# Kernel optimization log

Hardware: AMD Instinct MI355X
Metric: run time of the kernel (lower is better)

Reference implementation:

```python
import jax, jax.numpy as jnp
import numpy as np
import math

D_MODEL = 1024
EXPAND = 2
D_INNER = D_MODEL * EXPAND  # 2048
D_STATE = 16
DT_RANK = max(1, (D_MODEL + 15) // 16)  # 64
K = 4  # conv kernel size
B, S = 2, 2048


def silu(v):
    return v * jax.nn.sigmoid(v)


def setup_inputs() -> dict:
    key = jax.random.key(0)
    ks = jax.random.split(key, 12)
    sc = lambda fan_in: 1.0 / math.sqrt(fan_in)
    x = jax.random.normal(ks[0], (B, S, D_MODEL), dtype=jnp.float32)
    Win = jax.random.normal(ks[1], (D_MODEL, 2 * D_INNER), dtype=jnp.float32) * sc(D_MODEL)
    Wconv = jax.random.normal(ks[2], (D_INNER, 1, K), dtype=jnp.float32) * sc(K)
    bconv = jax.random.normal(ks[3], (D_INNER,), dtype=jnp.float32) * 0.01
    Wx = jax.random.normal(ks[4], (D_INNER, DT_RANK + 2 * D_STATE), dtype=jnp.float32) * sc(D_INNER)
    Wdt = jax.random.normal(ks[5], (DT_RANK, D_INNER), dtype=jnp.float32) * sc(DT_RANK)
    # dt_proj bias init: inverse-softplus of dt ~ LogUniform[1e-3, 1e-1]
    dt = jnp.exp(jax.random.uniform(ks[6], (D_INNER,)) * (math.log(0.1) - math.log(0.001)) + math.log(0.001))
    dt = jnp.clip(dt, 0.0001, None)
    bdt = dt + jnp.log(-jnp.expm1(-dt))
    a = jnp.arange(1, D_STATE + 1, dtype=jnp.float32)[None, :].repeat(D_INNER, axis=0)
    a = a + jax.random.uniform(ks[7], a.shape) * 0.1
    A_log = jnp.log(a)
    Dp = jnp.ones((D_INNER,), dtype=jnp.float32)
    Wout = jax.random.normal(ks[8], (D_INNER, D_MODEL), dtype=jnp.float32) * sc(D_INNER)
    return {"x": x, "Win": Win, "Wconv": Wconv, "bconv": bconv, "Wx": Wx,
            "Wdt": Wdt, "bdt": bdt, "A_log": A_log, "Dp": Dp, "Wout": Wout}


def causal_dw_conv(x, Wconv, bconv):
    # x: [B, S, C] -> depthwise causal conv along S
    xc = jnp.transpose(x, (0, 2, 1))  # [B, C, S]
    y = jax.lax.conv_general_dilated(
        xc, Wconv, window_strides=(1,), padding=[(K - 1, 0)],
        feature_group_count=D_INNER,
        dimension_numbers=("NCH", "OIH", "NCH"))
    y = y + bconv[None, :, None]
    return jnp.transpose(y, (0, 2, 1))  # [B, S, C]


def selective_scan(u, delta, b_term, c_term, A_log, Dp):
    # u, delta: [B,S,Di]; b_term, c_term: [B,S,Ds]
    a = -jnp.exp(A_log)  # [Di, Ds]
    delta_a = jnp.exp(delta[..., None] * a[None, None])            # [B,S,Di,Ds] fp32
    delta_b_u = (delta * u)[..., None] * b_term[:, :, None, :]     # [B,S,Di,Ds]
    du = u * Dp[None, None, :]                                     # [B,S,Di]
    # time-major for scan
    dA = jnp.transpose(delta_a, (1, 0, 2, 3))
    dBu = jnp.transpose(delta_b_u, (1, 0, 2, 3))
    c_t = jnp.transpose(c_term, (1, 0, 2))
    du_t = jnp.transpose(du, (1, 0, 2))

    def step(state, inp):
        dA_t, dBu_t, c, duv = inp
        state = dA_t * state + dBu_t                  # [B,Di,Ds]
        y = jnp.einsum("bdn,bn->bd", state, c) + duv  # [B,Di]
        return state, y

    init = jnp.zeros((u.shape[0], D_INNER, D_STATE), dtype=jnp.float32)
    _, ys = jax.lax.scan(step, init, (dA, dBu, c_t, du_t))
    return jnp.transpose(ys, (1, 0, 2))  # [B,S,Di]


def reference(x, Win, Wconv, bconv, Wx, Wdt, bdt, A_log, Dp, Wout):
    xz = x @ Win                              # [B,S,2*Di]
    x_branch, z_branch = jnp.split(xz, 2, axis=-1)
    x_branch = silu(causal_dw_conv(x_branch, Wconv, bconv))
    params = x_branch @ Wx                    # [B,S,R+2*Ds]
    delta, b_term, c_term = jnp.split(params, [DT_RANK, DT_RANK + D_STATE], axis=-1)
    delta = jax.nn.softplus(delta @ Wdt + bdt)
    y = selective_scan(x_branch, delta, b_term, c_term, A_log, Dp)
    y = y * silu(z_branch)
    return y @ Wout
```

## Files before the change

### kernel.cpp

```cpp
#include <hip/hip_runtime.h>

typedef unsigned short u16;
typedef _Float16 f16;
typedef f16 f16x8 __attribute__((ext_vector_type(8)));
typedef u16 u16x8 __attribute__((ext_vector_type(8)));
typedef short s16x8 __attribute__((ext_vector_type(8)));
typedef float f32x4 __attribute__((ext_vector_type(4)));
typedef float f32x8 __attribute__((ext_vector_type(8)));

#define T_TOK 4096
#define B_SZ 2
#define S_LEN 2048
#define DMODEL 1024
#define DI 2048
#define DS 16
#define RNK 64
#define NCH 64
#define CLEN 32
#define LDXZ 4096
#define SK 8
#define PRM_SLICE (4096 * 128)
#define LOG2E 1.4426950408889634f

#define GLOAD_LDS16(gp, lp)                                                                   \
  __builtin_amdgcn_global_load_lds((const __attribute__((address_space(1))) void*)(gp),       \
                                   (__attribute__((address_space(3))) void*)(lp), 16, 0, 0)

__device__ __forceinline__ float b2f(u16 v) { return __uint_as_float(((unsigned)v) << 16); }
__device__ __forceinline__ u16 f2b(float f) {
  unsigned u = __float_as_uint(f);
  return (u16)((u + 0x7fffu + ((u >> 16) & 1u)) >> 16);
}
__device__ __forceinline__ float fexp2(float x) {
#if __has_builtin(__builtin_amdgcn_exp2f)
  return __builtin_amdgcn_exp2f(x);
#else
  return exp2f(x);
#endif
}
__device__ __forceinline__ int dtype_of(const void* dp) {
  unsigned v = *(const unsigned*)dp;
  return (v == 0x3F800000u) ? 0 : (v == 0x3C003C00u) ? 2 : 1;
}
__device__ __forceinline__ float load_any(const void* p, size_t i, int flag) {
  if (flag == 0) return ((const float*)p)[i];
  if (flag == 1) return b2f(((const u16*)p)[i]);
  return (float)((const f16*)p)[i];
}

__device__ __forceinline__ void tr_tile(const void* __restrict__ src, void* __restrict__ dst,
                                        int R, int C, int Cpad, int f, int bx, int by, int ob) {
  __shared__ f16 t[32][33];
  int c0 = bx * 32, r0 = by * 32;
  int tx = threadIdx.x & 31, ty = threadIdx.x >> 5;
#pragma unroll
  for (int i = ty; i < 32; i += 8) {
    int r = r0 + i, c = c0 + tx;
    float v = (r < R && c < C) ? load_any(src, (size_t)r * C + c, f) : 0.f;
    t[i][tx] = (f16)v;
  }
  __syncthreads();
#pragma unroll
  for (int i = ty; i < 32; i += 8) {
    int c = c0 + i, r = r0 + tx;
    if (c < Cpad && r < R) {
      if (ob) ((u16*)dst)[(size_t)c * R + r] = f2b((float)t[tx][i]);
      else ((f16*)dst)[(size_t)c * R + r] = t[tx][i];
    }
  }
}

__global__ __launch_bounds__(256) void k_prep(const void* __restrict__ Wconv, const void* __restrict__ bconv,
                                              const void* __restrict__ bdt, const void* __restrict__ A_log,
                                              const void* __restrict__ Dp, const void* __restrict__ Wx,
                                              const void* __restrict__ Wdt, const void* __restrict__ Win,
                                              const void* __restrict__ x, f16* __restrict__ WxT,
                                              f16* __restrict__ WdtT, u16* __restrict__ WinTb,
                                              u16* __restrict__ xhb, float* __restrict__ a_f,
                                              float* __restrict__ wconv_f, float* __restrict__ bconv_f,
                                              float* __restrict__ bdt_f, float* __restrict__ dp_f,
                                              int* __restrict__ flag) {
  int f = dtype_of(Dp);
  int bid = blockIdx.x, t = threadIdx.x;
  if (bid < 128) {
    int i = bid * 256 + t;
    a_f[i] = -__expf(load_any(A_log, i, f)) * LOG2E;
  } else if (bid < 160) {
    int i = (bid - 128) * 256 + t;
    wconv_f[i] = load_any(Wconv, i, f);
  } else if (bid < 168) {
    int i = (bid - 160) * 256 + t;
    bconv_f[i] = load_any(bconv, i, f);
  } else if (bid < 176) {
    int i = (bid - 168) * 256 + t;
    bdt_f[i] = load_any(bdt, i, f);
  } else if (bid < 184) {
    int i = (bid - 176) * 256 + t;
    dp_f[i] = load_any(Dp, i, f);
  } else if (bid == 184) {
    if (t == 0) *flag = f;
  } else if (bid < 441) {
    int id = bid - 185;
    tr_tile(Wx, WxT, 2048, 96, 128, f, id & 3, id >> 2, 0);
  } else if (bid < 569) {
    int id = bid - 441;
    tr_tile(Wdt, WdtT, 64, 2048, 2048, f, id & 63, id >> 6, 0);
  } else if (bid < 4665) {
    int id = bid - 569;
    tr_tile(Win, WinTb, 1024, 4096, 4096, f, id & 127, id >> 7, 1);
  } else {
    if (f == 1) return;
    size_t i = (size_t)(bid - 4665) * 2048 + (size_t)t * 8;
    u16x8 o;
    if (f == 0) {
      const float* s = (const float*)x + i;
#pragma unroll
      for (int j = 0; j < 8; ++j) o[j] = f2b(s[j]);
    } else {
      const f16* s = (const f16*)x + i;
#pragma unroll
      for (int j = 0; j < 8; ++j) o[j] = f2b((float)s[j]);
    }
    *(u16x8*)(xhb + i) = o;
  }
}

__global__ __launch_bounds__(256) void k_transpose16(const void* __restrict__ src, f16* __restrict__ dst,
                                                     int R, int C, int Cpad, const void* __restrict__ Dp) {
  tr_tile(src, dst, R, C, Cpad, dtype_of(Dp), blockIdx.x, blockIdx.y, 0);
}

__global__ __launch_bounds__(512) void k_gemm1(const void* __restrict__ x0, const u16* __restrict__ xhb,
                                               const u16* __restrict__ Bw, f16* __restrict__ C,
                                               const int* __restrict__ flag) {
  constexpr int LD = 1024, LDC = LDXZ, NT = 16, NP = NT / 2;
  __shared__ __align__(16) u16 lds[8 * 8192];
  const u16* A = (*flag == 1) ? (const u16*)x0 : xhb;
  const int tid = threadIdx.x;
  const int wv = tid >> 6, ln = tid & 63;
  const int quad = ln >> 4, l16 = ln & 15;
  const int wr = wv >> 2, wc = wv & 3;
  const int m0 = blockIdx.y * 256, n0 = blockIdx.x * 256;
  const int rr = tid >> 3;
  const int cc = (tid & 7) ^ (rr & 7);
  const u16* aBase = A + (size_t)m0 * LD + cc * 8;
  const u16* bBase = Bw + (size_t)n0 * LD + cc * 8;
  const int brow = ((tid >> 8) << 6) + (rr & 31);
  u16* const dBase = lds + wv * 512;
  auto stageA = [&](int tile, int mq) {
    const u16* s = aBase + (size_t)(mq * 64 + rr) * LD + tile * 64;
    u16* d = dBase + ((tile & 1) * 4 + mq) * 8192;
    GLOAD_LDS16(s, d);
    GLOAD_LDS16(s + 128 * LD, d + 4096);
  };
  auto stageB = [&](int tile, int nq) {
    const u16* s = bBase + (size_t)(brow + nq * 32) * LD + tile * 64;
    u16* d = dBase + ((tile & 1) * 4 + 2 + nq) * 8192;
    GLOAD_LDS16(s, d);
    GLOAD_LDS16(s + 128 * LD, d + 4096);
  };
  const int rxor = (l16 & 7) << 3;
  f32x4 acc[8][4] = {};
  stageA(0, 0); stageB(0, 1); stageB(0, 0); stageA(0, 1);
  stageA(1, 0); stageB(1, 1);
  asm volatile("s_waitcnt vmcnt(4)" ::: "memory");
  __builtin_amdgcn_s_barrier();
  s16x8 af[4][2], bf[2][2];
  for (int pr = 0; pr < NP; ++pr) {
    const int t0 = 2 * pr;
    const bool more = (pr < NP - 1);
#pragma unroll
    for (int ph = 0; ph < 8; ++ph) {
      const int slot = ph >> 2, q = ph & 3;
      const int mq = q >> 1, nq = (q >> 1) ^ (q & 1);
      const u16* Ar = lds + (slot * 4 + mq) * 8192;
      const u16* Br = lds + (slot * 4 + 2 + nq) * 8192;
      if (q == 0 || q == 2) {
#pragma unroll
        for (int i = 0; i < 4; ++i) {
          const int ra = wr * 64 + i * 16 + l16;
#pragma unroll
          for (int kk = 0; kk < 2; ++kk)
            af[i][kk] = *(const s16x8*)(Ar + ra * 64 + ((kk * 32 + quad * 8) ^ rxor));
        }
      }
      if (q != 2) {
#pragma unroll
        for (int j = 0; j < 2; ++j) {
          const int rb = wc * 32 + j * 16 + l16;
#pragma unroll
          for (int kk = 0; kk < 2; ++kk)
            bf[j][kk] = *(const s16x8*)(Br + rb * 64 + ((kk * 32 + quad * 8) ^ rxor));
        }
      }
      if (ph == 0) stageB(t0 + 1, 0);
      else if (ph == 1) stageA(t0 + 1, 1);
      else if (more) {
        if (ph == 2) stageA(t0 + 2, 0);
        else if (ph == 3) stageB(t0 + 2, 1);
        else if (ph == 4) stageB(t0 + 2, 0);
        else if (ph == 5) stageA(t0 + 2, 1);
        else if (ph == 6) stageA(t0 + 3, 0);
        else stageB(t0 + 3, 1);
      }
      __builtin_amdgcn_s_barrier();
      asm volatile("s_waitcnt lgkmcnt(0)" ::: "memory");
      __builtin_amdgcn_sched_barrier(0);
      __builtin_amdgcn_s_setprio(1);
#pragma unroll
      for (int kk = 0; kk < 2; ++kk)
#pragma unroll
        for (int i = 0; i < 4; ++i)
#pragma unroll
          for (int j = 0; j < 2; ++j)
            acc[mq * 4 + i][nq * 2 + j] = __builtin_amdgcn_mfma_f32_16x16x32_bf16(
                af[i][kk], bf[j][kk], acc[mq * 4 + i][nq * 2 + j], 0, 0, 0);
      __builtin_amdgcn_s_setprio(0);
      if (ph == 3) {
        if (more) asm volatile("s_waitcnt vmcnt(6)" ::: "memory");
        else asm volatile("s_waitcnt vmcnt(2)" ::: "memory");
      } else if (ph == 5) {
        if (more) asm volatile("s_waitcnt vmcnt(8)" ::: "memory");
        else asm volatile("s_waitcnt vmcnt(0)" ::: "memory");
      } else if (ph == 7) {
        if (more) asm volatile("s_waitcnt vmcnt(4)" ::: "memory");
        else asm volatile("s_waitcnt vmcnt(0)" ::: "memory");
      }
      __builtin_amdgcn_s_barrier();
    }
  }
#pragma unroll
  for (int i = 0; i < 8; ++i)
#pragma unroll
    for (int j = 0; j < 4; ++j)
#pragma unroll
      for (int r = 0; r < 4; ++r) {
        const int row = m0 + wr * 128 + i * 16 + quad * 4 + r;
        const int col = n0 + wc * 64 + j * 16 + l16;
        C[(size_t)row * LDC + col] = (f16)acc[i][j][r];
      }
}

template <int BM, int BN, int EPI>
__global__ __launch_bounds__(256) void k_gemm2(const f16* __restrict__ A, const f16* __restrict__ B,
                                               void* __restrict__ Cv, const float* __restrict__ bias,
                                               const int* __restrict__ flag,
                                               int klen, int lda, int ldb, int ldc) {
  constexpr int WM = BM / 2, WN = BN / 2;
  constexpr int FM = WM / 16, FN = WN / 16;
  __shared__ __align__(16) f16 As[2 * BM * 32];
  __shared__ __align__(16) f16 Bs[2 * BN * 32];
  const int tid = threadIdx.x;
  const int wv = tid >> 6, ln = tid & 63;
  const int quad = ln >> 4, l16 = ln & 15;
  const int lrow = ln >> 2, lch = (ln & 3) * 8;
  const int m0 = blockIdx.y * BM, n0 = blockIdx.x * BN;
  const int wm = (wv & 1) * WM, wn = (wv >> 1) * WN;
  const int kbase = blockIdx.z * klen;
  f32x4 acc[FM][FN] = {};
  for (int kk = 0; kk < klen; kk += 64) {
    const int k0 = kbase + kk;
    __syncthreads();
#pragma unroll
    for (int h = 0; h < 2; ++h) {
#pragma unroll
      for (int i = 0; i < BM / 64; ++i) {
        int r0 = wv * (BM / 4) + i * 16;
        GLOAD_LDS16(A + (size_t)(m0 + r0 + lrow) * lda + k0 + h * 32 + lch, As + h * BM * 32 + r0 * 32);
      }
#pragma unroll
      for (int i = 0; i < BN / 64; ++i) {
        int r0 = wv * (BN / 4) + i * 16;
        GLOAD_LDS16(B + (size_t)(n0 + r0 + lrow) * ldb + k0 + h * 32 + lch, Bs + h * BN * 32 + r0 * 32);
      }
    }
    __syncthreads();
#pragma unroll
    for (int h = 0; h < 2; ++h) {
      f16x8 af[FM], bf[FN];
#pragma unroll
      for (int i = 0; i < FM; ++i) af[i] = *(const f16x8*)(As + h * BM * 32 + (wm + i * 16 + l16) * 32 + quad * 8);
#pragma unroll
      for (int j = 0; j < FN; ++j) bf[j] = *(const f16x8*)(Bs + h * BN * 32 + (wn + j * 16 + l16) * 32 + quad * 8);
#pragma unroll
      for (int i = 0; i < FM; ++i)
#pragma unroll
        for (int j = 0; j < FN; ++j)
          acc[i][j] = __builtin_amdgcn_mfma_f32_16x16x32_f16(af[i], bf[j], acc[i][j], 0, 0, 0);
    }
  }
  int dflag = 1;
  if constexpr (EPI == 2) dflag = *flag;
  f16* Cz = (f16*)Cv;
  if constexpr (EPI == 4) Cz = (f16*)Cv + (size_t)blockIdx.z * PRM_SLICE;
#pragma unroll
  for (int i = 0; i < FM; ++i)
#pragma unroll
    for (int j = 0; j < FN; ++j)
#pragma unroll
      for (int r = 0; r < 4; ++r) {
        int row = m0 + wm + i * 16 + quad * 4 + r;
        int col = n0 + wn + j * 16 + l16;
        size_t ci = (size_t)row * ldc + col;
        float v = acc[i][j][r];
        if constexpr (EPI == 3) {
          v += bias[row];
          v = (v > 20.f) ? v : log1pf(__expf(v));
          size_t di2 = ((size_t)(row << 1) + (col >> 11)) * (size_t)LDXZ + (col & 2047);
          Cz[di2] = (f16)v;
        } else if constexpr (EPI == 2) {
          if (dflag == 0) ((float*)Cv)[ci] = v;
          else if (dflag == 1) ((u16*)Cv)[ci] = f2b(v);
          else ((f16*)Cv)[ci] = (f16)v;
        } else {
          Cz[ci] = (f16)v;
        }
      }
}

__global__ __launch_bounds__(256) void k_sum_prm(const f16* __restrict__ parts, f16* __restrict__ prm,
                                                 float* __restrict__ prmBC) {
  size_t i = (size_t)(blockIdx.x * 256 + threadIdx.x) * 8;
  int col0 = (int)(i & 127);
  if (col0 >= 96) return;
  float s[8] = {};
#pragma unroll
  for (int z = 0; z < SK; ++z) {
    f16x8 v = *(const f16x8*)(parts + (size_t)z * PRM_SLICE + i);
#pragma unroll
    for (int j = 0; j < 8; ++j) s[j] += (float)v[j];
  }
  if (col0 < 64) {
    f16x8 o;
#pragma unroll
    for (int j = 0; j < 8; ++j) o[j] = (f16)s[j];
    *(f16x8*)(prm + i) = o;
  } else {
    size_t tok = i >> 7;
    f32x8 of;
#pragma unroll
    for (int j = 0; j < 8; ++j) of[j] = s[j];
    *(f32x8*)(prmBC + tok * 32 + (col0 - 64)) = of;
  }
}

__global__ __launch_bounds__(256) void k_conv_silu(const f16* __restrict__ xz, const float* __restrict__ Wconv,
                                                   const float* __restrict__ bconv, f16* __restrict__ xc) {
  int t = blockIdx.x;
  int s = t & (S_LEN - 1);
  int d8 = threadIdx.x * 8;
  float w[4][8];
#pragma unroll
  for (int i = 0; i < 8; ++i)
#pragma unroll
    for (int j = 0; j < 4; ++j) w[j][i] = Wconv[(d8 + i) * 4 + j];
  float acc[8];
#pragma unroll
  for (int i = 0; i < 8; ++i) acc[i] = bconv[d8 + i];
#pragma unroll
  for (int j = 0; j < 4; ++j) {
    int sl = s - 3 + j;
    if (sl >= 0) {
      f16x8 xv = *(const f16x8*)(xz + (size_t)(t - 3 + j) * LDXZ + d8);
#pragma unroll
      for (int i = 0; i < 8; ++i) acc[i] = fmaf((float)xv[i], w[j][i], acc[i]);
    }
  }
  f16x8 o;
#pragma unroll
  for (int i = 0; i < 8; ++i) {
    float v = acc[i];
    o[i] = (f16)(v / (1.f + __expf(-v)));
  }
  *(f16x8*)(xc + (size_t)t * DI + d8) = o;
}

__global__ __launch_bounds__(256) void k_scan_passA(const f16* __restrict__ dltT, const f16* __restrict__ u,
                                                    const float* __restrict__ prmBC, const float* __restrict__ a_f,
                                                    f16* __restrict__ lcs, float* __restrict__ sumdv) {
  int g = blockIdx.x * 256 + threadIdx.x;
  int nh = g & 1, p = g >> 1;
  int d = p & (DI - 1);
  int c = (p >> 11) & (NCH - 1);
  int b = p >> 17;
  f32x4 a0 = *(const f32x4*)(a_f + d * DS + nh * 8);
  f32x4 a1 = *(const f32x4*)(a_f + d * DS + nh * 8 + 4);
  float a[8] = {a0[0], a0[1], a0[2], a0[3], a1[0], a1[1], a1[2], a1[3]};
  int t0 = b * S_LEN + c * CLEN;
  const f16* dp = dltT + (size_t)(2 * d + b) * LDXZ + c * CLEN;
  const f16* up = u + (size_t)t0 * DI + d;
  const float* bp = prmBC + (size_t)t0 * 32 + nh * 8;
  f16x8 dlv[4];
#pragma unroll
  for (int q = 0; q < 4; ++q) dlv[q] = *(const f16x8*)(dp + q * 8);
  float uf[4];
#pragma unroll
  for (int q = 0; q < 4; ++q) uf[q] = (float)up[(size_t)q * DI];
  f32x8 bvv[2];
#pragma unroll
  for (int q = 0; q < 2; ++q) bvv[q] = *(const f32x8*)(bp + q * 32);
  float st[8] = {};
  float sumd = 0.f;
#pragma unroll
  for (int s = 0; s < CLEN; ++s) {
    float dl = (float)dlv[s >> 3][s & 7];
    float uv = uf[s & 3];
    f32x8 bv = bvv[s & 1];
    if (s + 4 < CLEN) uf[s & 3] = (float)up[(size_t)(s + 4) * DI];
    if (s + 2 < CLEN) bvv[s & 1] = *(const f32x8*)(bp + (s + 2) * 32);
    sumd += dl;
    float dbu = dl * uv;
#pragma unroll
    for (int j = 0; j < 8; ++j) {
      float e = fexp2(dl * a[j]);
      st[j] = fmaf(e, st[j], dbu * bv[j]);
    }
  }
  f16x8 o;
#pragma unroll
  for (int j = 0; j < 8; ++j) o[j] = (f16)st[j];
  *(f16x8*)(lcs + (size_t)p * DS + nh * 8) = o;
  if (nh == 0) sumdv[p] = sumd;
}

__global__ __launch_bounds__(256) void k_scan_passB(f16* __restrict__ lcs, const float* __restrict__ sumdv,
                                                    const float* __restrict__ a_f) {
  int g = blockIdx.x * 256 + threadIdx.x;
  int n = g & 15, d = (g >> 4) & (DI - 1), b = g >> 15;
  float an = a_f[d * DS + n];
  const size_t base = (size_t)b * NCH * DI + d;
  float lf[4], sf[4];
#pragma unroll
  for (int q = 0; q < 4; ++q) {
    size_t pq = base + (size_t)q * DI;
    lf[q] = (float)lcs[pq * DS + n];
    sf[q] = sumdv[pq];
  }
  float init = 0.f;
#pragma unroll
  for (int c = 0; c < NCH; ++c) {
    size_t pc = base + (size_t)c * DI;
    float l = lf[c & 3], sd = sf[c & 3];
    if (c + 4 < NCH) {
      size_t pn = base + (size_t)(c + 4) * DI;
      lf[c & 3] = (float)lcs[pn * DS + n];
      sf[c & 3] = sumdv[pn];
    }
    lcs[pc * DS + n] = (f16)init;
    init = fexp2(sd * an) * init + l;
  }
}

__global__ __launch_bounds__(256) void k_scan_passC(const f16* __restrict__ dltT, const f16* __restrict__ u,
                                                    const float* __restrict__ prmBC, const float* __restrict__ a_f,
                                                    const float* __restrict__ dp_f, const f16* __restrict__ lcs,
                                                    f16* __restrict__ xz) {
  int g = blockIdx.x * 256 + threadIdx.x;
  int nh = g & 1, p = g >> 1;
  int d = p & (DI - 1);
  int c = (p >> 11) & (NCH - 1);
  int b = p >> 17;
  f32x4 a0 = *(const f32x4*)(a_f + d * DS + nh * 8);
  f32x4 a1 = *(const f32x4*)(a_f + d * DS + nh * 8 + 4);
  float a[8] = {a0[0], a0[1], a0[2], a0[3], a1[0], a1[1], a1[2], a1[3]};
  float st[8];
  f16x8 iv = *(const f16x8*)(lcs + (size_t)p * DS + nh * 8);
#pragma unroll
  for (int j = 0; j < 8; ++j) st[j] = (float)iv[j];
  float dpv = dp_f[d];
  int t0 = b * S_LEN + c * CLEN;
  const f16* dp = dltT + (size_t)(2 * d + b) * LDXZ + c * CLEN;
  const f16* up = u + (size_t)t0 * DI + d;
  const float* bp = prmBC + (size_t)t0 * 32 + nh * 8;
  f16* zp = xz + (size_t)t0 * LDXZ + DI + d;
  f16x8 dlv[4];
#pragma unroll
  for (int q = 0; q < 4; ++q) dlv[q] = *(const f16x8*)(dp + q * 8);
  float uf[4], zf[4];
#pragma unroll
  for (int q = 0; q < 4; ++q) {
    uf[q] = (float)up[(size_t)q * DI];
    zf[q] = (float)zp[(size_t)q * LDXZ];
  }
  f32x8 bvv[2], cvv[2];
#pragma unroll
  for (int q = 0; q < 2; ++q) {
    bvv[q] = *(const f32x8*)(bp + q * 32);
    cvv[q] = *(const f32x8*)(bp + q * 32 + 16);
  }
#pragma unroll
  for (int s = 0; s < CLEN; ++s) {
    float dl = (float)dlv[s >> 3][s & 7];
    float uv = uf[s & 3];
    float z = zf[s & 3];
    f32x8 bv = bvv[s & 1];
    f32x8 cv = cvv[s & 1];
    if (s + 4 < CLEN) {
      uf[s & 3] = (float)up[(size_t)(s + 4) * DI];
      zf[s & 3] = (float)zp[(size_t)(s + 4) * LDXZ];
    }
    if (s + 2 < CLEN) {
      bvv[s & 1] = *(const f32x8*)(bp + (s + 2) * 32);
      cvv[s & 1] = *(const f32x8*)(bp + (s + 2) * 32 + 16);
    }
    float dbu = dl * uv;
    float part = (nh == 0) ? uv * dpv : 0.f;
#pragma unroll
    for (int j = 0; j < 8; ++j) {
      float e = fexp2(dl * a[j]);
      st[j] = fmaf(e, st[j], dbu * bv[j]);
      part = fmaf(st[j], cv[j], part);
    }
    part += __shfl_xor(part, 1, 64);
    if (nh == 0) {
      float sg = 1.f / (1.f + __expf(-z));
      zp[(size_t)s * LDXZ] = (f16)(part * z * sg);
    }
  }
}

extern "C" void kernel_launch(void* const* d_in, const int* in_sizes, int n_in,
                              void* d_out, int out_size, void* d_ws, size_t ws_size,
                              hipStream_t stream) {
  const void* x = d_in[0];
  const void* Win = d_in[1];
  const void* Wconv = d_in[2];
  const void* bconv = d_in[3];
  const void* Wx = d_in[4];
  const void* Wdt = d_in[5];
  const void* bdt = d_in[6];
  const void* A_log = d_in[7];
  const void* Dp = d_in[8];
  const void* Wout = d_in[9];
  (void)in_sizes; (void)n_in; (void)out_size; (void)ws_size;

  const size_t KB = 1024, MB = 1024 * 1024;
  char* ws = (char*)d_ws;
  f16* xzh = (f16*)ws;
  u16* xhb = (u16*)(ws + 32 * MB);
  f16* xch = (f16*)(ws + 32 * MB);
  u16* WinTb = (u16*)(ws + 48 * MB);
  f16* parts = (f16*)(ws + 48 * MB);
  f16* lcs = (f16*)(ws + 48 * MB);
  f16* WoutT = (f16*)(ws + 48 * MB);
  float* sumd = (float*)(ws + 56 * MB);
  f16* prm = (f16*)(ws + 57 * MB);
  float* prmBC = (float*)(ws + 58 * MB);
  f16* WxT = (f16*)(ws + 58 * MB + 512 * KB);
  f16* WdtT = (f16*)(ws + 59 * MB);
  float* a_f = (float*)(ws + 59 * MB + 256 * KB);
  float* wconv_f = (float*)(ws + 59 * MB + 384 * KB);
  float* bconv_f = (float*)(ws + 59 * MB + 416 * KB);
  float* bdt_f = (float*)(ws + 59 * MB + 424 * KB);
  float* dp_f = (float*)(ws + 59 * MB + 432 * KB);
  int* flag = (int*)(ws + 59 * MB + 440 * KB);

  k_prep<<<6713, 256, 0, stream>>>(Wconv, bconv, bdt, A_log, Dp, Wx, Wdt, Win, x,
                                   WxT, WdtT, WinTb, xhb, a_f, wconv_f, bconv_f, bdt_f, dp_f, flag);

  k_gemm1<<<dim3(16, 16), 512, 0, stream>>>(x, xhb, WinTb, xzh, flag);
  k_conv_silu<<<T_TOK, 256, 0, stream>>>(xzh, wconv_f, bconv_f, xch);
  k_gemm2<64, 128, 4><<<dim3(1, 4096 / 64, SK), 256, 0, stream>>>(
      xch, WxT, parts, nullptr, flag, 2048 / SK, 2048, 2048, 128);
  k_sum_prm<<<PRM_SLICE / 8 / 256, 256, 0, stream>>>(parts, prm, prmBC);
  k_gemm2<128, 128, 3><<<dim3(4096 / 128, 2048 / 128), 256, 0, stream>>>(
      WdtT, prm, xzh, bdt_f, flag, 64, 64, 128, 0);
  k_scan_passA<<<(B_SZ * NCH * DI * 2) / 256, 256, 0, stream>>>(xzh, xch, prmBC, a_f, lcs, sumd);
  k_scan_passB<<<(B_SZ * DI * DS) / 256, 256, 0, stream>>>(lcs, sumd, a_f);
  k_scan_passC<<<(B_SZ * NCH * DI * 2) / 256, 256, 0, stream>>>(xzh, xch, prmBC, a_f, dp_f, lcs, xzh);
  k_transpose16<<<dim3(1024 / 32, 2048 / 32), 256, 0, stream>>>(Wout, WoutT, 2048, 1024, 1024, Dp);
  k_gemm2<64, 128, 2><<<dim3(1024 / 128, 4096 / 64), 256, 0, stream>>>(
      xzh + DI, WoutT, d_out, nullptr, flag, 2048, LDXZ, 2048, 1024);
}
```

Measured before the change: 343.3 us.

## Stage scan chunk inputs and gated output through LDS with vectorized loads

Scan passes A and C now cooperatively load each block's u, z and B/C tiles for a chunk into shared memory with 16-byte vector loads, replacing per-thread strided 2-byte global loads. Pass C also writes the gated output into LDS and then stores it back with coalesced vector writes. This targets the poor coalescing of the per-timestep scalar loads and stores. In exchange it adds barriers, LDS usage and a serialized load phase that no longer overlaps with compute through the register prefetch pipeline.

```diff
diff --git a/kernel.cpp b/kernel.cpp
--- a/kernel.cpp
+++ b/kernel.cpp
@@ -5,6 +5,7 @@
 typedef f16 f16x8 __attribute__((ext_vector_type(8)));
 typedef u16 u16x8 __attribute__((ext_vector_type(8)));
 typedef short s16x8 __attribute__((ext_vector_type(8)));
+typedef float f32x2 __attribute__((ext_vector_type(2)));
 typedef float f32x4 __attribute__((ext_vector_type(4)));
 typedef float f32x8 __attribute__((ext_vector_type(8)));
 
@@ -378,42 +379,52 @@
 __global__ __launch_bounds__(256) void k_scan_passA(const f16* __restrict__ dltT, const f16* __restrict__ u,
                                                     const float* __restrict__ prmBC, const float* __restrict__ a_f,
                                                     f16* __restrict__ lcs, float* __restrict__ sumdv) {
-  int g = blockIdx.x * 256 + threadIdx.x;
+  __shared__ __align__(16) f16 u_lds[CLEN][128];
+  __shared__ __align__(16) float b_lds[CLEN][16];
+  const int tid = threadIdx.x;
+  int g = blockIdx.x * 256 + tid;
   int nh = g & 1, p = g >> 1;
   int d = p & (DI - 1);
   int c = (p >> 11) & (NCH - 1);
   int b = p >> 17;
+  const int d0 = d & ~127;
+  const int t0 = b * S_LEN + c * CLEN;
+  {
+    const f16* up0 = u + (size_t)t0 * DI + d0;
+#pragma unroll
+    for (int rep = 0; rep < 2; ++rep) {
+      int chunk = rep * 256 + tid;
+      int row = chunk >> 4, c16 = chunk & 15;
+      *(f16x8*)&u_lds[row][c16 * 8] = *(const f16x8*)(up0 + (size_t)row * DI + c16 * 8);
+    }
+    const float* bp0 = prmBC + (size_t)t0 * 32;
+    int row = tid >> 3, c2 = tid & 7;
+    *(f32x2*)&b_lds[row][c2 * 2] = *(const f32x2*)(bp0 + row * 32 + c2 * 2);
+  }
+  const f16* dp = dltT + (size_t)(2 * d + b) * LDXZ + c * CLEN;
+  f16x8 dlv[4];
+#pragma unroll
+  for (int q = 0; q < 4; ++q) dlv[q] = *(const f16x8*)(dp + q * 8);
   f32x4 a0 = *(const f32x4*)(a_f + d * DS + nh * 8);
   f32x4 a1 = *(const f32x4*)(a_f + d * DS + nh * 8 + 4);
   float a[8] = {a0[0], a0[1], a0[2], a0[3], a1[0], a1[1], a1[2], a1[3]};
-  int t0 = b * S_LEN + c * CLEN;
-  const f16* dp = dltT + (size_t)(2 * d + b) * LDXZ + c * CLEN;
-  const f16* up = u + (size_t)t0 * DI + d;
-  const float* bp = prmBC + (size_t)t0 * 32 + nh * 8;
-  f16x8 dlv[4];
-#pragma unroll
-  for (int q = 0; q < 4; ++q) dlv[q] = *(const f16x8*)(dp + q * 8);
-  float uf[4];
-#pragma unroll
-  for (int q = 0; q < 4; ++q) uf[q] = (float)up[(size_t)q * DI];
-  f32x8 bvv[2];
-#pragma unroll
-  for (int q = 0; q < 2; ++q) bvv[q] = *(const f32x8*)(bp + q * 32);
+  __syncthreads();
+  const int dd = d - d0;
   float st[8] = {};
   float sumd = 0.f;
 #pragma unroll
   for (int s = 0; s < CLEN; ++s) {
     float dl = (float)dlv[s >> 3][s & 7];
-    float uv = uf[s & 3];
-    f32x8 bv = bvv[s & 1];
-    if (s + 4 < CLEN) uf[s & 3] = (float)up[(size_t)(s + 4) * DI];
-    if (s + 2 < CLEN) bvv[s & 1] = *(const f32x8*)(bp + (s + 2) * 32);
+    float uv = (float)u_lds[s][dd];
+    f32x4 bv0 = *(const f32x4*)&b_lds[s][nh * 8];
+    f32x4 bv1 = *(const f32x4*)&b_lds[s][nh * 8 + 4];
     sumd += dl;
     float dbu = dl * uv;
 #pragma unroll
     for (int j = 0; j < 8; ++j) {
       float e = fexp2(dl * a[j]);
-      st[j] = fmaf(e, st[j], dbu * bv[j]);
+      float bj = (j < 4) ? bv0[j & 3] : bv1[j & 3];
+      st[j] = fmaf(e, st[j], dbu * bj);
     }
   }
   f16x8 o;
@@ -455,11 +466,33 @@
                                                     const float* __restrict__ prmBC, const float* __restrict__ a_f,
                                                     const float* __restrict__ dp_f, const f16* __restrict__ lcs,
                                                     f16* __restrict__ xz) {
-  int g = blockIdx.x * 256 + threadIdx.x;
+  __shared__ __align__(16) f16 u_lds[CLEN][128];
+  __shared__ __align__(16) f16 z_lds[CLEN][128];
+  __shared__ __align__(16) float bc_lds[CLEN][32];
+  const int tid = threadIdx.x;
+  int g = blockIdx.x * 256 + tid;
   int nh = g & 1, p = g >> 1;
   int d = p & (DI - 1);
   int c = (p >> 11) & (NCH - 1);
   int b = p >> 17;
+  const int d0 = d & ~127;
+  const int t0 = b * S_LEN + c * CLEN;
+  f16* const zp0 = xz + (size_t)t0 * LDXZ + DI + d0;
+  {
+    const f16* up0 = u + (size_t)t0 * DI + d0;
+#pragma unroll
+    for (int rep = 0; rep < 2; ++rep) {
+      int chunk = rep * 256 + tid;
+      int row = chunk >> 4, c16 = chunk & 15;
+      *(f16x8*)&u_lds[row][c16 * 8] = *(const f16x8*)(up0 + (size_t)row * DI + c16 * 8);
+      *(f16x8*)&z_lds[row][c16 * 8] = *(const f16x8*)(zp0 + (size_t)row * LDXZ + c16 * 8);
+    }
+    ((f32x4*)bc_lds)[tid] = ((const f32x4*)(prmBC + (size_t)t0 * 32))[tid];
+  }
+  const f16* dp = dltT + (size_t)(2 * d + b) * LDXZ + c * CLEN;
+  f16x8 dlv[4];
+#pragma unroll
+  for (int q = 0; q < 4; ++q) dlv[q] = *(const f16x8*)(dp + q * 8);
   f32x4 a0 = *(const f32x4*)(a_f + d * DS + nh * 8);
   f32x4 a1 = *(const f32x4*)(a_f + d * DS + nh * 8 + 4);
   float a[8] = {a0[0], a0[1], a0[2], a0[3], a1[0], a1[1], a1[2], a1[3]};
@@ -468,54 +501,39 @@
 #pragma unroll
   for (int j = 0; j < 8; ++j) st[j] = (float)iv[j];
   float dpv = dp_f[d];
-  int t0 = b * S_LEN + c * CLEN;
-  const f16* dp = dltT + (size_t)(2 * d + b) * LDXZ + c * CLEN;
-  const f16* up = u + (size_t)t0 * DI + d;
-  const float* bp = prmBC + (size_t)t0 * 32 + nh * 8;
-  f16* zp = xz + (size_t)t0 * LDXZ + DI + d;
-  f16x8 dlv[4];
-#pragma unroll
-  for (int q = 0; q < 4; ++q) dlv[q] = *(const f16x8*)(dp + q * 8);
-  float uf[4], zf[4];
-#pragma unroll
-  for (int q = 0; q < 4; ++q) {
-    uf[q] = (float)up[(size_t)q * DI];
-    zf[q] = (float)zp[(size_t)q * LDXZ];
-  }
-  f32x8 bvv[2], cvv[2];
-#pragma unroll
-  for (int q = 0; q < 2; ++q) {
-    bvv[q] = *(const f32x8*)(bp + q * 32);
-    cvv[q] = *(const f32x8*)(bp + q * 32 + 16);
-  }
+  __syncthreads();
+  const int dd = d - d0;
 #pragma unroll
   for (int s = 0; s < CLEN; ++s) {
     float dl = (float)dlv[s >> 3][s & 7];
-    float uv = uf[s & 3];
-    float z = zf[s & 3];
-    f32x8 bv = bvv[s & 1];
-    f32x8 cv = cvv[s & 1];
-    if (s + 4 < CLEN) {
-      uf[s & 3] = (float)up[(size_t)(s + 4) * DI];
-      zf[s & 3] = (float)zp[(size_t)(s + 4) * LDXZ];
-    }
-    if (s + 2 < CLEN) {
-      bvv[s & 1] = *(const f32x8*)(bp + (s + 2) * 32);
-      cvv[s & 1] = *(const f32x8*)(bp + (s + 2) * 32 + 16);
-    }
+    float uv = (float)u_lds[s][dd];
+    float z = (float)z_lds[s][dd];
+    f32x4 bv0 = *(const f32x4*)&bc_lds[s][nh * 8];
+    f32x4 bv1 = *(const f32x4*)&bc_lds[s][nh * 8 + 4];
+    f32x4 cv0 = *(const f32x4*)&bc_lds[s][16 + nh * 8];
+    f32x4 cv1 = *(const f32x4*)&bc_lds[s][16 + nh * 8 + 4];
     float dbu = dl * uv;
     float part = (nh == 0) ? uv * dpv : 0.f;
 #pragma unroll
     for (int j = 0; j < 8; ++j) {
       float e = fexp2(dl * a[j]);
-      st[j] = fmaf(e, st[j], dbu * bv[j]);
-      part = fmaf(st[j], cv[j], part);
+      float bj = (j < 4) ? bv0[j & 3] : bv1[j & 3];
+      float cj = (j < 4) ? cv0[j & 3] : cv1[j & 3];
+      st[j] = fmaf(e, st[j], dbu * bj);
+      part = fmaf(st[j], cj, part);
     }
     part += __shfl_xor(part, 1, 64);
     if (nh == 0) {
       float sg = 1.f / (1.f + __expf(-z));
-      zp[(size_t)s * LDXZ] = (f16)(part * z * sg);
-    }
+      z_lds[s][dd] = (f16)(part * z * sg);
+    }
+  }
+  __syncthreads();
+#pragma unroll
+  for (int rep = 0; rep < 2; ++rep) {
+    int chunk = rep * 256 + tid;
+    int row = chunk >> 4, c16 = chunk & 15;
+    *(f16x8*)(zp0 + (size_t)row * LDXZ + c16 * 8) = *(const f16x8*)&z_lds[row][c16 * 8];
   }
 }
 
```

Result: faster. 324.4 us (-5.5%).
